# Performance work log

Hardware: AMD Instinct MI355X
Metric: run time of the kernel (lower is better)

## Reference

```python
import jax, jax.numpy as jnp
import numpy as np

B, J, O = 32, 20, 20
D, H, F, L = 256, 8, 1024, 6
S = J * O
DH = D // H
NL = L + 1  # 6 encoder blocks + final block stacked together


def setup_inputs() -> dict:
    ks = jax.random.split(jax.random.key(0), 16)
    s = 0.02
    am = jax.random.randint(ks[4], (B, J), 0, 2) == 1
    am = am.at[:, 0].set(False)  # at least one unmasked job per row (avoid all -inf softmax)
    return {
        "operations": jax.random.normal(ks[0], (B, J, O, 2), jnp.float32),
        "job_ops_mask": jax.random.normal(ks[1], (B, J, O, O), jnp.float32),
        "ops_machines_mask": jax.random.normal(ks[2], (B, S, S), jnp.float32),
        "jobs_next_op_idx": jax.random.randint(ks[3], (B, J, 1), 0, O),
        "action_mask": am,
        "qkv_w": jax.random.normal(ks[5], (NL, 3 * D, D), jnp.float32) * s,
        "qkv_b": jnp.zeros((NL, 3 * D), jnp.float32),
        "out_w": jax.random.normal(ks[6], (NL, D, D), jnp.float32) * s,
        "out_b": jnp.zeros((NL, D), jnp.float32),
        "ln1_g": jnp.ones((NL, D), jnp.float32),
        "ln1_b": jnp.zeros((NL, D), jnp.float32),
        "ln2_g": jnp.ones((NL, D), jnp.float32),
        "ln2_b": jnp.zeros((NL, D), jnp.float32),
        "ff1_w": jax.random.normal(ks[7], (NL, F, D), jnp.float32) * s,
        "ff1_b": jnp.zeros((NL, F), jnp.float32),
        "ff2_w": jax.random.normal(ks[8], (NL, D, F), jnp.float32) * s,
        "ff2_b": jnp.zeros((NL, D), jnp.float32),
        "op_emb_w": jax.random.normal(ks[9], (D, 2), jnp.float32) * s,
        "op_emb_b": jnp.zeros((D,), jnp.float32),
        "pol_w": jax.random.normal(ks[10], (1, D), jnp.float32) * s,
        "pol_b": jnp.zeros((1,), jnp.float32),
    }


def _ln(x, g, b):
    m = x.mean(-1, keepdims=True)
    v = ((x - m) ** 2).mean(-1, keepdims=True)
    return (x - m) * jax.lax.rsqrt(v + 1e-5) * g + b


def _mha(x, mask, qw, qb, ow, ob):
    N, Sq, _ = x.shape
    qkv = x @ qw.T + qb
    q, k, v = jnp.split(qkv, 3, axis=-1)
    q = q.reshape(N, Sq, H, DH).transpose(0, 2, 1, 3)
    k = k.reshape(N, Sq, H, DH).transpose(0, 2, 1, 3)
    v = v.reshape(N, Sq, H, DH).transpose(0, 2, 1, 3)
    sc = jnp.einsum("nhqd,nhkd->nhqk", q, k) / jnp.sqrt(jnp.float32(DH))
    sc = sc + mask  # additive float attn mask, broadcast over heads where needed
    a = jax.nn.softmax(sc, axis=-1)
    o = jnp.einsum("nhqk,nhkd->nhqd", a, v).transpose(0, 2, 1, 3).reshape(N, Sq, D)
    return o @ ow.T + ob


def _forward(operations, job_ops_mask, ops_machines_mask, jobs_next_op_idx, action_mask,
             qkv_w, qkv_b, out_w, out_b, ln1_g, ln1_b, ln2_g, ln2_b,
             ff1_w, ff1_b, ff2_w, ff2_b, op_emb_w, op_emb_b, pol_w, pol_b):
    def block(x, mask, i):  # pre-norm TransformerEncoderLayer, gelu, dropout=0
        h = _ln(x, ln1_g[i], ln1_b[i])
        x = x + _mha(h, mask, qkv_w[i], qkv_b[i], out_w[i], out_b[i])
        h = _ln(x, ln2_g[i], ln2_b[i])
        ff = jax.nn.gelu(h @ ff1_w[i].T + ff1_b[i], approximate=False) @ ff2_w[i].T + ff2_b[i]
        return x + ff

    # sinusoidal positional encoding over the operation index
    pos = jnp.arange(O, dtype=jnp.float32)[:, None]
    div = jnp.exp(jnp.arange(0, D, 2, dtype=jnp.float32) * (-np.log(10000.0) / D))
    pe = jnp.stack([jnp.sin(pos * div), jnp.cos(pos * div)], axis=-1).reshape(O, D)
    x = operations @ op_emb_w.T + op_emb_b + pe[None, None]  # (B,J,O,D)

    # ALiBi slopes: 1/x^(i+1), x = 256^(1/H)
    base = (2.0 ** 8) ** (1.0 / H)
    slope = (1.0 / base ** jnp.arange(1, H + 1, dtype=jnp.float32))[None, :, None, None]
    job_mask = job_ops_mask.reshape(B * J, 1, O, O) * slope  # (B*J, H, O, O)
    mach_mask = ops_machines_mask[:, None, :, :]  # (B, 1, S, S), identical across heads

    for i in range(L):
        if i % 2 == 0:  # per-job attention over operations
            x = block(x.reshape(B * J, O, D), job_mask, i).reshape(B, J, O, D)
        else:  # per-machine attention over all operations
            x = block(x.reshape(B, S, D), mach_mask, i).reshape(B, J, O, D)

    idx = jnp.broadcast_to(jobs_next_op_idx[:, :, :, None], (B, J, 1, D))
    nxt = jnp.take_along_axis(x, idx, axis=2)[:, :, 0, :]  # (B, J, D)
    kp = jnp.where(action_mask, -jnp.inf, 0.0)[:, None, None, :]  # key padding mask
    nxt = block(nxt, kp, L)
    logits = (nxt @ pol_w.T + pol_b)[:, :, 0]
    return jnp.where(action_mask, -jnp.inf, logits)


def reference(operations, job_ops_mask, ops_machines_mask, jobs_next_op_idx, action_mask,
              qkv_w, qkv_b, out_w, out_b, ln1_g, ln1_b, ln2_g, ln2_b,
              ff1_w, ff1_b, ff2_w, ff2_b, op_emb_w, op_emb_b, pol_w, pol_b):
    return _forward(operations, job_ops_mask, ops_machines_mask, jobs_next_op_idx, action_mask,
                    qkv_w, qkv_b, out_w, out_b, ln1_g, ln1_b, ln2_g, ln2_b,
                    ff1_w, ff1_b, ff2_w, ff2_b, op_emb_w, op_emb_b, pol_w, pol_b)
```

## Files before the change

kernel.cpp:

```cpp
#include <hip/hip_runtime.h>
#include <math.h>

#define B_  32
#define J_  20
#define O_  20
#define S_  400
#define D_  256
#define H_  8
#define F_  1024
#define L_  6
#define T_  12800
#define T2_ 640

#define NEG_BIG (-1e30f)

typedef __attribute__((ext_vector_type(8))) short short8;
typedef __attribute__((ext_vector_type(4))) float f32x4;

__device__ __forceinline__ short f2b(float f) {
  union { float f; unsigned u; } c; c.f = f;
  unsigned r = (c.u + 0x7FFFu + ((c.u >> 16) & 1u)) >> 16;
  return (short)r;
}
__device__ __forceinline__ float b2f(short s) {
  union { unsigned u; float f; } c;
  c.u = ((unsigned)(unsigned short)s) << 16;
  return c.f;
}
__device__ __forceinline__ unsigned addpk(unsigned a, unsigned b) {
  union { unsigned u; float f; } x, y;
  x.u = a << 16;        y.u = b << 16;        float lo = x.f + y.f;
  x.u = a & 0xffff0000u; y.u = b & 0xffff0000u; float hi = x.f + y.f;
  return (unsigned)(unsigned short)f2b(lo) | ((unsigned)(unsigned short)f2b(hi) << 16);
}
__device__ __forceinline__ void async_copy16(const short* g, short* l) {
  __builtin_amdgcn_global_load_lds(
      (const __attribute__((address_space(1))) void*)g,
      (__attribute__((address_space(3))) void*)l, 16, 0, 0);
}

__global__ __launch_bounds__(256) void k_f2b4(
    const float* __restrict__ s0, short* __restrict__ d0,
    const float* __restrict__ s1, short* __restrict__ d1,
    const float* __restrict__ s2, short* __restrict__ d2,
    const float* __restrict__ s3, short* __restrict__ d3,
    const float* __restrict__ s4, short* __restrict__ d4)
{
  int bid = blockIdx.x;
  const float* src; short* dst; int base;
  if (bid < 672)        { src = s0; dst = d0; base = bid; }
  else if (bid < 896)   { src = s1; dst = d1; base = bid - 672; }
  else if (bid < 1792)  { src = s2; dst = d2; base = bid - 896; }
  else if (bid < 2688)  { src = s3; dst = d3; base = bid - 1792; }
  else                  { src = s4; dst = d4; base = bid - 2688; }
  int i = (base * 256 + threadIdx.x) * 8;
  float4 a = *(const float4*)(src + i);
  float4 b = *(const float4*)(src + i + 4);
  short8 o;
  o[0] = f2b(a.x); o[1] = f2b(a.y); o[2] = f2b(a.z); o[3] = f2b(a.w);
  o[4] = f2b(b.x); o[5] = f2b(b.y); o[6] = f2b(b.z); o[7] = f2b(b.w);
  *(short8*)(dst + i) = o;
}

__global__ __launch_bounds__(640) void k_maskconv(
    const void* __restrict__ am_raw, int* __restrict__ am_out)
{
  __shared__ int isInt32;
  const int tid = threadIdx.x;
  if (tid == 0) isInt32 = 1;
  __syncthreads();
  if (tid < 160) {
    int v = ((const int*)am_raw)[tid];
    if (v != 0 && v != 1) atomicAnd(&isInt32, 0);
  }
  __syncthreads();
  if (tid < 640) {
    int v;
    if (isInt32) v = ((const int*)am_raw)[tid] != 0;
    else         v = ((const unsigned char*)am_raw)[tid] != 0;
    am_out[tid] = v;
  }
}

__global__ __launch_bounds__(256) void k_embed(
    const float* __restrict__ ops, const float* __restrict__ ew,
    const float* __restrict__ eb, short* __restrict__ x)
{
  int idx = blockIdx.x * 256 + threadIdx.x;
  int d = idx & 255;
  int t = idx >> 8;
  int o = t % O_;
  float a0 = ops[(size_t)t * 2 + 0], a1 = ops[(size_t)t * 2 + 1];
  int k = d >> 1;
  float div = expf((float)(2 * k) * -0.03597789207803197f);
  float ang = (float)o * div;
  float pe = (d & 1) ? cosf(ang) : sinf(ang);
  x[idx] = f2b(a0 * ew[d * 2 + 0] + a1 * ew[d * 2 + 1] + eb[d] + pe);
}

__global__ __launch_bounds__(256) void k_ln(
    const short* __restrict__ x, const float* __restrict__ g, const float* __restrict__ b,
    short* __restrict__ out, int nTok)
{
  int gid = blockIdx.x * 256 + threadIdx.x;
  int tok = gid >> 6, lane = threadIdx.x & 63;
  if (tok >= nTok) return;
  int2 pk = ((const int2*)(x + (size_t)tok * 256))[lane];
  union { unsigned u; float f; } c;
  float vx, vy, vz, vw;
  c.u = (unsigned)pk.x << 16;        vx = c.f;
  c.u = (unsigned)pk.x & 0xffff0000u; vy = c.f;
  c.u = (unsigned)pk.y << 16;        vz = c.f;
  c.u = (unsigned)pk.y & 0xffff0000u; vw = c.f;
  float s = vx + vy + vz + vw;
  #pragma unroll
  for (int off = 32; off > 0; off >>= 1) s += __shfl_down(s, off);
  float mean = __shfl(s, 0) * (1.f / 256.f);
  float dx = vx - mean, dy = vy - mean, dz = vz - mean, dw = vw - mean;
  float q = dx * dx + dy * dy + dz * dz + dw * dw;
  #pragma unroll
  for (int off = 32; off > 0; off >>= 1) q += __shfl_down(q, off);
  float var = __shfl(q, 0) * (1.f / 256.f);
  float inv = 1.f / sqrtf(var + 1e-5f);
  float4 gv = ((const float4*)g)[lane];
  float4 bv = ((const float4*)b)[lane];
  float ox = dx * inv * gv.x + bv.x;
  float oy = dy * inv * gv.y + bv.y;
  float oz = dz * inv * gv.z + bv.z;
  float ow = dw * inv * gv.w + bv.w;
  int2 po;
  po.x = (int)(unsigned short)f2b(ox) | ((int)(unsigned short)f2b(oy) << 16);
  po.y = (int)(unsigned short)f2b(oz) | ((int)(unsigned short)f2b(ow) << 16);
  ((int2*)(out + (size_t)tok * 256))[lane] = po;
}

__global__ __launch_bounds__(256) void k_gemm_bf16(
    const short* __restrict__ A, const short* __restrict__ W,
    const float* __restrict__ bias, const short* __restrict__ R,
    short* __restrict__ C, int M, int N, int K, int act)
{
  __shared__ short LDS_[32768];
  short* Csf = LDS_;
  const int tid  = threadIdx.x;
  const int lane = tid & 63;
  const int wv   = tid >> 6;
  const int lm   = lane & 15;
  const int quad = lane >> 4;
  const int wm   = (wv >> 1) * 64;
  const int wn   = (wv & 1) * 64;
  const int n0 = blockIdx.x * 128;
  const int m0 = blockIdx.y * 128;

  f32x4 acc[4][4] = {};

#define GB_STAGE(buf, kk)                                                      \
  { _Pragma("unroll")                                                          \
    for (int i = 0; i < 4; ++i) {                                              \
      const int c    = tid + 256 * i;                       \
      const int row  = c >> 3;                                     \
      const int kc8  = ((c & 7) ^ (row & 7)) * 8;                              \
      async_copy16(A + (size_t)(m0 + row) * K + (kk) + kc8,                    \
                   &LDS_[(buf) * 16384 + c * 8]);                              \
      async_copy16(W + (size_t)(n0 + row) * K + (kk) + kc8,                    \
                   &LDS_[(buf) * 16384 + 8192 + c * 8]);                       \
    } }

  GB_STAGE(0, 0)
  __syncthreads();

  const int nIter = K >> 6;
  for (int t = 0; t < nIter; ++t) {
    const int cur = t & 1;
    if (t + 1 < nIter) GB_STAGE(cur ^ 1, (t + 1) << 6)
    const short* Asf = &LDS_[cur * 16384];
    const short* Bsf = &LDS_[cur * 16384 + 8192];
    #pragma unroll
    for (int kh = 0; kh < 2; ++kh) {
      short8 af[4], bf[4];
      #pragma unroll
      for (int i = 0; i < 4; ++i) {
        const int row  = wm + i * 16 + lm;
        const int slot = (kh * 4 + quad) ^ (lm & 7);
        af[i] = *(short8*)&Asf[(row * 8 + slot) * 8];
      }
      #pragma unroll
      for (int j = 0; j < 4; ++j) {
        const int row  = wn + j * 16 + lm;
        const int slot = (kh * 4 + quad) ^ (lm & 7);
        bf[j] = *(short8*)&Bsf[(row * 8 + slot) * 8];
      }
      #pragma unroll
      for (int i = 0; i < 4; ++i)
        #pragma unroll
        for (int j = 0; j < 4; ++j)
          acc[i][j] = __builtin_amdgcn_mfma_f32_16x16x32_bf16(af[i], bf[j], acc[i][j], 0, 0, 0);
    }
    __syncthreads();
  }
#undef GB_STAGE

  #pragma unroll
  for (int j = 0; j < 4; ++j) {
    const int ccol = wn + j * 16 + lm;
    const float bv = bias[n0 + ccol];
    #pragma unroll
    for (int i = 0; i < 4; ++i) {
      #pragma unroll
      for (int r = 0; r < 4; ++r) {
        const int row = wm + i * 16 + quad * 4 + r;
        float vvv = acc[i][j][r] + bv;
        if (act) vvv = vvv / (1.f + __expf(-1.702f * vvv));
        Csf[row * 136 + ccol] = f2b(vvv);
      }
    }
  }
  __syncthreads();
  {
    const int srow = tid >> 1, sh = (tid & 1) * 64;
    const size_t gbase = (size_t)(m0 + srow) * N + n0 + sh;
    const short* ls = &Csf[srow * 136 + sh];
    #pragma unroll
    for (int u = 0; u < 8; ++u) {
      uint4 v = *(const uint4*)(ls + u * 8);
      if (R) {
        uint4 rv = *(const uint4*)(R + gbase + u * 8);
        v.x = addpk(v.x, rv.x); v.y = addpk(v.y, rv.y);
        v.z = addpk(v.z, rv.z); v.w = addpk(v.w, rv.w);
      }
      *(uint4*)(C + gbase + u * 8) = v;
    }
  }
}

__global__ __launch_bounds__(256) void k_gemm_ln(
    const short* __restrict__ A, const short* __restrict__ W,
    const float* __restrict__ bias, const short* __restrict__ R,
    short* __restrict__ X, short* __restrict__ Hout,
    const float* __restrict__ g, const float* __restrict__ bb_,
    int M, int K)
{
  __shared__ short LDS_[40960];
  short* Csf = LDS_;
  const int tid  = threadIdx.x;
  const int lane = tid & 63;
  const int wv   = tid >> 6;
  const int lm   = lane & 15;
  const int quad = lane >> 4;
  const int wn   = wv * 64;
  const int m0   = blockIdx.x * 64;

  f32x4 acc[4][4] = {};

#define GL_STAGE(buf, kk)                                                      \
  { _Pragma("unroll")                                                          \
    for (int i = 0; i < 2; ++i) {                           \
      const int c   = tid + 256 * i;                                           \
      const int row = c >> 3;                                                  \
      const int kc8 = ((c & 7) ^ (row & 7)) * 8;                               \
      async_copy16(A + (size_t)(m0 + row) * K + (kk) + kc8,                    \
                   &LDS_[(buf) * 20480 + c * 8]);                              \
    }                                                                          \
    _Pragma("unroll")                                                          \
    for (int i = 0; i < 8; ++i) {           \
      const int c   = tid + 256 * i;                                           \
      const int row = c >> 3;                                                  \
      const int kc8 = ((c & 7) ^ (row & 7)) * 8;                               \
      async_copy16(W + (size_t)row * K + (kk) + kc8,                           \
                   &LDS_[(buf) * 20480 + 4096 + c * 8]);                       \
    } }

  GL_STAGE(0, 0)
  __syncthreads();

  const int nIter = K >> 6;
  for (int t = 0; t < nIter; ++t) {
    const int cur = t & 1;
    if (t + 1 < nIter) GL_STAGE(cur ^ 1, (t + 1) << 6)
    const short* Asf = &LDS_[cur * 20480];
    const short* Bsf = &LDS_[cur * 20480 + 4096];
    #pragma unroll
    for (int kh = 0; kh < 2; ++kh) {
      short8 af[4], bf[4];
      #pragma unroll
      for (int i = 0; i < 4; ++i) {
        const int row  = i * 16 + lm;
        const int slot = (kh * 4 + quad) ^ (lm & 7);
        af[i] = *(short8*)&Asf[(row * 8 + slot) * 8];
      }
      #pragma unroll
      for (int j = 0; j < 4; ++j) {
        const int row  = wn + j * 16 + lm;
        const int slot = (kh * 4 + quad) ^ (lm & 7);
        bf[j] = *(short8*)&Bsf[(row * 8 + slot) * 8];
      }
      #pragma unroll
      for (int i = 0; i < 4; ++i)
        #pragma unroll
        for (int j = 0; j < 4; ++j)
          acc[i][j] = __builtin_amdgcn_mfma_f32_16x16x32_bf16(af[i], bf[j], acc[i][j], 0, 0, 0);
    }
    __syncthreads();
  }
#undef GL_STAGE

  #pragma unroll
  for (int j = 0; j < 4; ++j) {
    const int ccol = wn + j * 16 + lm;
    const float bv = bias[ccol];
    #pragma unroll
    for (int i = 0; i < 4; ++i) {
      #pragma unroll
      for (int r = 0; r < 4; ++r) {
        const int row = i * 16 + quad * 4 + r;
        Csf[row * 264 + ccol] = f2b(acc[i][j][r] + bv);
      }
    }
  }
  __syncthreads();

  {
    const int row = tid >> 2, cb = (tid & 3) * 64;
    const size_t gbase = (size_t)(m0 + row) * 256 + cb;
    const short* ls = &Csf[row * 264 + cb];
    uint4 xv[8];
    float s1 = 0.f, s2 = 0.f;
    #pragma unroll
    for (int u = 0; u < 8; ++u) {
      uint4 v = *(const uint4*)(ls + u * 8);
      uint4 rv = *(const uint4*)(R + gbase + u * 8);
      v.x = addpk(v.x, rv.x); v.y = addpk(v.y, rv.y);
      v.z = addpk(v.z, rv.z); v.w = addpk(v.w, rv.w);
      xv[u] = v;
      *(uint4*)(X + gbase + u * 8) = v;
      #pragma unroll
      for (int w2 = 0; w2 < 4; ++w2) {
        unsigned pv = (&v.x)[w2];
        union { unsigned u; float f; } c1, c2;
        c1.u = pv << 16; c2.u = pv & 0xffff0000u;
        s1 += c1.f + c2.f;
        s2 += c1.f * c1.f + c2.f * c2.f;
      }
    }
    s1 += __shfl_xor(s1, 1); s2 += __shfl_xor(s2, 1);
    s1 += __shfl_xor(s1, 2); s2 += __shfl_xor(s2, 2);
    const float mean = s1 * (1.f / 256.f);
    const float var  = s2 * (1.f / 256.f) - mean * mean;
    const float inv  = 1.f / sqrtf(var + 1e-5f);
    #pragma unroll
    for (int u = 0; u < 8; ++u) {
      float4 g0 = *(const float4*)(g + cb + u * 8);
      float4 g1 = *(const float4*)(g + cb + u * 8 + 4);
      float4 b0 = *(const float4*)(bb_ + cb + u * 8);
      float4 b1 = *(const float4*)(bb_ + cb + u * 8 + 4);
      auto lnpk = [&](unsigned pv, float ga, float gb2, float ba, float bb2) -> unsigned {
        union { unsigned u; float f; } c1, c2;
        c1.u = pv << 16; c2.u = pv & 0xffff0000u;
        float lo = (c1.f - mean) * inv * ga + ba;
        float hi = (c2.f - mean) * inv * gb2 + bb2;
        return (unsigned)(unsigned short)f2b(lo) | ((unsigned)(unsigned short)f2b(hi) << 16);
      };
      uint4 hv;
      hv.x = lnpk(xv[u].x, g0.x, g0.y, b0.x, b0.y);
      hv.y = lnpk(xv[u].y, g0.z, g0.w, b0.z, b0.w);
      hv.z = lnpk(xv[u].z, g1.x, g1.y, b1.x, b1.y);
      hv.w = lnpk(xv[u].w, g1.z, g1.w, b1.z, b1.w);
      *(uint4*)(Hout + gbase + u * 8) = hv;
    }
  }
}

#define QSTR 776
#define PSTR20 40
__global__ __launch_bounds__(512) void k_attn20_mfma(
    const short* __restrict__ qkv, short* __restrict__ att,
    const float* __restrict__ jmask, const int* __restrict__ amask, int mode)
{
  __shared__ short QK[32 * QSTR];
  __shared__ short Ps[8][32 * PSTR20];
  const int seq  = blockIdx.x;
  const int tid  = threadIdx.x;
  const int wv   = tid >> 6;
  const int lane = tid & 63;
  const int l15  = lane & 15;
  const int quad = lane >> 4;
  const float scale = 0.1767766952966369f;

  for (int e = tid; e < 3072; e += 512) {
    int row = e / 96, c8 = (e % 96) * 8;
    uint4 v = {0u, 0u, 0u, 0u};
    if (row < 20) v = *(const uint4*)(qkv + ((size_t)seq * 20 + row) * 768 + c8);
    *(uint4*)&QK[row * QSTR + c8] = v;
  }
  __syncthreads();

  const short8 aq0 = *(short8*)&QK[(0  + l15) * QSTR + wv * 32 + quad * 8];
  const short8 aq1 = *(short8*)&QK[(16 + l15) * QSTR + wv * 32 + quad * 8];
  const short8 bk0 = *(short8*)&QK[(0  + l15) * QSTR + 256 + wv * 32 + quad * 8];
  const short8 bk1 = *(short8*)&QK[(16 + l15) * QSTR + 256 + wv * 32 + quad * 8];
  f32x4 z4 = {0.f, 0.f, 0.f, 0.f};
  f32x4 s00 = __builtin_amdgcn_mfma_f32_16x16x32_bf16(aq0, bk0, z4, 0, 0, 0);
  f32x4 s01 = __builtin_amdgcn_mfma_f32_16x16x32_bf16(aq0, bk1, z4, 0, 0, 0);
  f32x4 s10 = __builtin_amdgcn_mfma_f32_16x16x32_bf16(aq1, bk0, z4, 0, 0, 0);
  f32x4 s11 = __builtin_amdgcn_mfma_f32_16x16x32_bf16(aq1, bk1, z4, 0, 0, 0);

  const float slope = exp2f(-(float)(wv + 1));
  short* psw = &Ps[wv][0];
  float l0[4] = {0.f, 0.f, 0.f, 0.f};
  float l1[4] = {0.f, 0.f, 0.f, 0.f};

  #pragma unroll
  for (int kt = 0; kt < 2; ++kt) {
    const int k  = kt * 16 + l15;
    const int kc = (k < 20) ? k : 19;
    float madd1 = 0.f;
    if (mode == 1) madd1 = amask[seq * 20 + kc] ? NEG_BIG : 0.f;
    #pragma unroll
    for (int qt = 0; qt < 2; ++qt) {
      f32x4 s = (kt == 0) ? (qt == 0 ? s00 : s10) : (qt == 0 ? s01 : s11);
      #pragma unroll
      for (int r = 0; r < 4; ++r) {
        const int q  = qt * 16 + quad * 4 + r;
        const int qc = (q < 20) ? q : 19;
        float sv = s[r] * scale;
        if (mode == 0) sv += jmask[(size_t)seq * 400 + qc * 20 + kc] * slope;
        else           sv += madd1;
        float p = (k < 20) ? __expf(fminf(sv, 40.f)) : 0.f;
        if (qt == 0) l0[r] += p; else l1[r] += p;
        psw[q * PSTR20 + k] = f2b(p);
      }
    }
  }
  #pragma unroll
  for (int r = 0; r < 4; ++r) {
    float t0 = l0[r];
    t0 += __shfl_xor(t0, 1); t0 += __shfl_xor(t0, 2);
    t0 += __shfl_xor(t0, 4); t0 += __shfl_xor(t0, 8);
    l0[r] = 1.f / t0;
    float t1 = l1[r];
    t1 += __shfl_xor(t1, 1); t1 += __shfl_xor(t1, 2);
    t1 += __shfl_xor(t1, 4); t1 += __shfl_xor(t1, 8);
    l1[r] = 1.f / t1;
  }

  const short8 pf0 = *(short8*)&psw[(0  + l15) * PSTR20 + quad * 8];
  const short8 pf1 = *(short8*)&psw[(16 + l15) * PSTR20 + quad * 8];
  #pragma unroll
  for (int dt = 0; dt < 2; ++dt) {
    const int d = wv * 32 + dt * 16 + l15;
    short8 vf;
    #pragma unroll
    for (int j = 0; j < 8; ++j)
      vf[j] = QK[(quad * 8 + j) * QSTR + 512 + d];
    f32x4 o0 = __builtin_amdgcn_mfma_f32_16x16x32_bf16(pf0, vf, z4, 0, 0, 0);
    f32x4 o1 = __builtin_amdgcn_mfma_f32_16x16x32_bf16(pf1, vf, z4, 0, 0, 0);
    #pragma unroll
    for (int r = 0; r < 4; ++r) {
      const int q = quad * 4 + r;
      att[((size_t)seq * 20 + q) * 256 + d] = f2b(o0[r] * l0[r]);
    }
    if (quad == 0) {
      #pragma unroll
      for (int r = 0; r < 4; ++r) {
        const int q = 16 + r;
        att[((size_t)seq * 20 + q) * 256 + d] = f2b(o1[r] * l1[r]);
      }
    }
  }
}

#define VTS 416
__global__ __launch_bounds__(256) void k_vtrans(
    const short* __restrict__ qkv, short* __restrict__ vt)
{
  __shared__ short T[64][73];
  const int bid = blockIdx.x;
  const int b  = bid / 28, rem = bid % 28;
  const int kt = rem / 4, dt = rem % 4;
  const int k0 = kt * 64, d0 = dt * 64;
  const int tid = threadIdx.x;
  #pragma unroll
  for (int i = 0; i < 2; ++i) {
    const int c = tid + 256 * i;
    const int row = c >> 3, cc = (c & 7) * 8;
    const int tok = k0 + row;
    uint4 v = {0u, 0u, 0u, 0u};
    if (tok < 400)
      v = *(const uint4*)(qkv + ((size_t)(b * 400 + tok)) * 768 + 512 + d0 + cc);
    *(uint4*)&T[row][cc] = v;
  }
  __syncthreads();
  #pragma unroll
  for (int i = 0; i < 2; ++i) {
    const int c = tid + 256 * i;
    const int dl = c >> 3, kk = (c & 7) * 8;
    if (k0 + kk < VTS) {
      short8 o;
      #pragma unroll
      for (int j = 0; j < 8; ++j) o[j] = T[kk + j][dl];
      *(short8*)(vt + ((size_t)(b * 256 + d0 + dl)) * VTS + k0 + kk) = o;
    }
  }
}

#define KSTR  36
#define VSTRL 436
#define PSTRW 40
__global__ __launch_bounds__(512) void k_attn400_mfma(
    const short* __restrict__ qkv, const short* __restrict__ vt,
    short* __restrict__ att, const short* __restrict__ mbf)
{
  __shared__ short Kl[416 * KSTR];
  __shared__ short Vl[32 * VSTRL];
  __shared__ short Pl[8][2 * 16 * PSTRW];

  const int id   = blockIdx.x;
  const int b    = id & 31;
  const int hd   = id >> 5;
  const int tid  = threadIdx.x;
  const int wv   = tid >> 6;
  const int lane = tid & 63;
  const int l15  = lane & 15;
  const int quad = lane >> 4;
  const float scale = 0.1767766952966369f;

  const short* qbase = qkv + (size_t)b * 400 * 768;
  const short* kgl   = qbase + 256 + hd * 32;
  const short* vtb   = vt + ((size_t)b * 256 + hd * 32) * VTS;

  for (int e = tid; e < 1664; e += 512) {
    const int row = e >> 2, seg = e & 3;
    const int rs = row < 400 ? row : 399;
    uint4 v = *(const uint4*)(kgl + (size_t)rs * 768 + seg * 8);
    *(uint4*)&Kl[row * KSTR + seg * 8] = v;
  }
  for (int e = tid; e < 1664; e += 512) {
    const int row = e / 52, seg = e % 52;
    uint4 v = *(const uint4*)(vtb + (size_t)row * VTS + seg * 8);
    *(uint4*)&Vl[row * VSTRL + seg * 8] = v;
  }
  __syncthreads();

  short* Pw0 = &Pl[wv][0];
  short* Pw1 = &Pl[wv][16 * PSTRW];

  for (int tile = wv; tile < 13; tile += 8) {
    const int q0 = tile * 32;
    const short8 af0 = *(const short8*)(qbase + (size_t)(q0 + l15) * 768 + hd * 32 + quad * 8);
    int aq1 = q0 + 16 + l15; if (aq1 > 399) aq1 = 399;
    const short8 af1 = *(const short8*)(qbase + (size_t)aq1 * 768 + hd * 32 + quad * 8);
    const short* mr0 = mbf + (size_t)(b * 400 + q0 + l15) * 400;
    const short* mr1 = mbf + (size_t)(b * 400 + aq1) * 400;

    f32x4 accO[2][2] = {};
    float lsum0 = 0.f, lsum1 = 0.f;

    #pragma unroll
    for (int k0 = 0; k0 < 416; k0 += 32) {
      const short8 kf0 = *(const short8*)&Kl[(k0 + l15) * KSTR + quad * 8];
      const short8 kf1 = *(const short8*)&Kl[(k0 + 16 + l15) * KSTR + quad * 8];
      f32x4 z4 = {0.f, 0.f, 0.f, 0.f};
      f32x4 s00 = __builtin_amdgcn_mfma_f32_16x16x32_bf16(kf0, af0, z4, 0, 0, 0);
      f32x4 s01 = __builtin_amdgcn_mfma_f32_16x16x32_bf16(kf1, af0, z4, 0, 0, 0);
      f32x4 s10 = __builtin_amdgcn_mfma_f32_16x16x32_bf16(kf0, af1, z4, 0, 0, 0);
      f32x4 s11 = __builtin_amdgcn_mfma_f32_16x16x32_bf16(kf1, af1, z4, 0, 0, 0);

      uint2 ma0 = *(const uint2*)(mr0 + k0 + quad * 4);
      uint2 mb0 = *(const uint2*)(mr0 + k0 + 16 + quad * 4);
      uint2 ma1 = *(const uint2*)(mr1 + k0 + quad * 4);
      uint2 mb1 = *(const uint2*)(mr1 + k0 + 16 + quad * 4);

      float p00[4], p01[4], p10[4], p11[4];
      #pragma unroll
      for (int r = 0; r < 4; ++r) {
        const int kB = k0 + 16 + quad * 4 + r;
        union { unsigned u; float f; } cm;
        unsigned wa0 = (r < 2) ? ma0.x : ma0.y;
        unsigned wb0 = (r < 2) ? mb0.x : mb0.y;
        unsigned wa1 = (r < 2) ? ma1.x : ma1.y;
        unsigned wb1 = (r < 2) ? mb1.x : mb1.y;
        cm.u = (r & 1) ? (wa0 & 0xffff0000u) : (wa0 << 16); float mA0 = cm.f;
        cm.u = (r & 1) ? (wb0 & 0xffff0000u) : (wb0 << 16); float mB0 = cm.f;
        cm.u = (r & 1) ? (wa1 & 0xffff0000u) : (wa1 << 16); float mA1 = cm.f;
        cm.u = (r & 1) ? (wb1 & 0xffff0000u) : (wb1 << 16); float mB1 = cm.f;
        float sA0 = s00[r] * scale + mA0;
        float sB0 = (kB < 400) ? (s01[r] * scale + mB0) : NEG_BIG;
        float sA1 = s10[r] * scale + mA1;
        float sB1 = (kB < 400) ? (s11[r] * scale + mB1) : NEG_BIG;
        p00[r] = __expf(fminf(sA0, 40.f));
        p01[r] = __expf(fminf(sB0, 40.f));
        p10[r] = __expf(fminf(sA1, 40.f));
        p11[r] = __expf(fminf(sB1, 40.f));
        lsum0 += p00[r] + p01[r];
        lsum1 += p10[r] + p11[r];
      }

      unsigned q00, q01, q02, q03, q10, q11, q12, q13;
      asm("v_cvt_pk_bf16_f32 %0, %1, %2" : "=v"(q00) : "v"(p00[0]), "v"(p00[1]));
      asm("v_cvt_pk_bf16_f32 %0, %1, %2" : "=v"(q01) : "v"(p00[2]), "v"(p00[3]));
      asm("v_cvt_pk_bf16_f32 %0, %1, %2" : "=v"(q02) : "v"(p01[0]), "v"(p01[1]));
      asm("v_cvt_pk_bf16_f32 %0, %1, %2" : "=v"(q03) : "v"(p01[2]), "v"(p01[3]));
      asm("v_cvt_pk_bf16_f32 %0, %1, %2" : "=v"(q10) : "v"(p10[0]), "v"(p10[1]));
      asm("v_cvt_pk_bf16_f32 %0, %1, %2" : "=v"(q11) : "v"(p10[2]), "v"(p10[3]));
      asm("v_cvt_pk_bf16_f32 %0, %1, %2" : "=v"(q12) : "v"(p11[0]), "v"(p11[1]));
      asm("v_cvt_pk_bf16_f32 %0, %1, %2" : "=v"(q13) : "v"(p11[2]), "v"(p11[3]));
      uint2 w00; w00.x = q00; w00.y = q01;
      uint2 w01; w01.x = q02; w01.y = q03;
      uint2 w10; w10.x = q10; w10.y = q11;
      uint2 w11; w11.x = q12; w11.y = q13;
      *(uint2*)&Pw0[l15 * PSTRW + quad * 4]      = w00;
      *(uint2*)&Pw0[l15 * PSTRW + 16 + quad * 4] = w01;
      *(uint2*)&Pw1[l15 * PSTRW + quad * 4]      = w10;
      *(uint2*)&Pw1[l15 * PSTRW + 16 + quad * 4] = w11;
      const short8 pf0 = *(short8*)&Pw0[l15 * PSTRW + quad * 8];
      const short8 pf1 = *(short8*)&Pw1[l15 * PSTRW + quad * 8];

      const short8 vf0 = *(const short8*)&Vl[l15 * VSTRL + k0 + quad * 8];
      const short8 vf1 = *(const short8*)&Vl[(16 + l15) * VSTRL + k0 + quad * 8];
      accO[0][0] = __builtin_amdgcn_mfma_f32_16x16x32_bf16(vf0, pf0, accO[0][0], 0, 0, 0);
      accO[0][1] = __builtin_amdgcn_mfma_f32_16x16x32_bf16(vf1, pf0, accO[0][1], 0, 0, 0);
      accO[1][0] = __builtin_amdgcn_mfma_f32_16x16x32_bf16(vf0, pf1, accO[1][0], 0, 0, 0);
      accO[1][1] = __builtin_amdgcn_mfma_f32_16x16x32_bf16(vf1, pf1, accO[1][1], 0, 0, 0);
    }

    lsum0 += __shfl_xor(lsum0, 16);
    lsum0 += __shfl_xor(lsum0, 32);
    lsum1 += __shfl_xor(lsum1, 16);
    lsum1 += __shfl_xor(lsum1, 32);
    const float inv0 = 1.f / lsum0;
    const float inv1 = 1.f / lsum1;

    #pragma unroll
    for (int qh = 0; qh < 2; ++qh) {
      const int q = q0 + qh * 16 + l15;
      if (q >= 400) continue;
      const float inv = qh ? inv1 : inv0;
      #pragma unroll
      for (int c = 0; c < 2; ++c) {
        float a0 = accO[qh][c][0] * inv, a1 = accO[qh][c][1] * inv;
        float a2 = accO[qh][c][2] * inv, a3 = accO[qh][c][3] * inv;
        unsigned o01, o23;
        asm("v_cvt_pk_bf16_f32 %0, %1, %2" : "=v"(o01) : "v"(a0), "v"(a1));
        asm("v_cvt_pk_bf16_f32 %0, %1, %2" : "=v"(o23) : "v"(a2), "v"(a3));
        uint2 ov; ov.x = o01; ov.y = o23;
        *(uint2*)&att[((size_t)b * 400 + q) * 256 + hd * 32 + c * 16 + quad * 4] = ov;
      }
    }
  }
}

__global__ __launch_bounds__(256) void k_gather2(
    const short* __restrict__ x, const short* __restrict__ h,
    const int* __restrict__ idx, short* __restrict__ x2, short* __restrict__ h2)
{
  int t = blockIdx.x * 256 + threadIdx.x;
  if (t >= 640 * 16) return;
  int bj = t >> 4, c = t & 15;
  int o = idx[bj];
  size_t src = ((size_t)bj * 20 + o) * 256;
  ((uint4*)(x2 + (size_t)bj * 256))[c] = ((const uint4*)(x + src))[c];
  ((uint4*)(h2 + (size_t)bj * 256))[c] = ((const uint4*)(h + src))[c];
}

__global__ __launch_bounds__(256) void k_logits(
    const short* __restrict__ x2, const float* __restrict__ pw, const float* __restrict__ pb,
    const int* __restrict__ am, float* __restrict__ out)
{
  int gid = blockIdx.x * 256 + threadIdx.x;
  int row = gid >> 6, lane = threadIdx.x & 63;
  int2 pk = ((const int2*)(x2 + (size_t)row * 256))[lane];
  union { unsigned u; float f; } c;
  float vx, vy, vz, vw;
  c.u = (unsigned)pk.x << 16;         vx = c.f;
  c.u = (unsigned)pk.x & 0xffff0000u; vy = c.f;
  c.u = (unsigned)pk.y << 16;         vz = c.f;
  c.u = (unsigned)pk.y & 0xffff0000u; vw = c.f;
  float4 w = ((const float4*)pw)[lane];
  float s = vx * w.x + vy * w.y + vz * w.z + vw * w.w;
  #pragma unroll
  for (int off = 32; off > 0; off >>= 1) s += __shfl_down(s, off);
  if (lane == 0) out[row] = am[row] ? NEG_BIG : (s + pb[0]);
}

extern "C" void kernel_launch(void* const* d_in, const int* in_sizes, int n_in,
                              void* d_out, int out_size, void* d_ws, size_t ws_size,
                              hipStream_t stream)
{
  (void)in_sizes; (void)n_in; (void)out_size; (void)ws_size;
  const float* operations        = (const float*)d_in[0];
  const float* job_ops_mask      = (const float*)d_in[1];
  const float* ops_machines_mask = (const float*)d_in[2];
  const int*   jobs_next_op_idx  = (const int*)d_in[3];
  const void*  action_mask_raw   = (const void*)d_in[4];
  const float* qkv_w = (const float*)d_in[5];
  const float* qkv_b = (const float*)d_in[6];
  const float* out_w = (const float*)d_in[7];
  const float* out_b = (const float*)d_in[8];
  const float* ln1_g = (const float*)d_in[9];
  const float* ln1_b = (const float*)d_in[10];
  const float* ln2_g = (const float*)d_in[11];
  const float* ln2_b = (const float*)d_in[12];
  const float* ff1_w = (const float*)d_in[13];
  const float* ff1_b = (const float*)d_in[14];
  const float* ff2_w = (const float*)d_in[15];
  const float* ff2_b = (const float*)d_in[16];
  const float* op_emb_w = (const float*)d_in[17];
  const float* op_emb_b = (const float*)d_in[18];
  const float* pol_w = (const float*)d_in[19];
  const float* pol_b = (const float*)d_in[20];
  float* out = (float*)d_out;

  short* x    = (short*)d_ws;
  short* x2   = x + (size_t)T_ * D_;
  short* h    = x2 + (size_t)T2_ * D_;
  short* big  = h + (size_t)T_ * D_;
  short* h2   = big + (size_t)T_ * F_;
  short* big2 = h2 + (size_t)T2_ * D_;
  int*   amc  = (int*)(big2 + (size_t)T2_ * F_);
  short* bwq  = (short*)(amc + 640);
  short* bwo  = bwq + (size_t)7 * 768 * 256;
  short* bwf1 = bwo + (size_t)7 * 256 * 256;
  short* bwf2 = bwf1 + (size_t)7 * 1024 * 256;
  short* mbf  = bwf2 + (size_t)7 * 256 * 1024;
  short* vt   = mbf + (size_t)B_ * 400 * 400;

  auto gemm = [&](const short* A, const short* Wb, const float* bias, const short* R,
                  short* C, int M, int N, int K, int act) {
    k_gemm_bf16<<<dim3(N / 128, M / 128), dim3(256), 0, stream>>>(
        A, Wb, bias, R, C, M, N, K, act);
  };
  auto gemm_ln = [&](const short* A, const short* Wb, const float* bias, const short* R,
                     short* X, short* Hout, const float* g, const float* b, int M, int K) {
    k_gemm_ln<<<dim3(M / 64), dim3(256), 0, stream>>>(
        A, Wb, bias, R, X, Hout, g, b, M, K);
  };

  k_f2b4<<<dim3(5188), 256, 0, stream>>>(qkv_w, bwq, out_w, bwo, ff1_w, bwf1,
                                         ff2_w, bwf2, ops_machines_mask, mbf);
  k_maskconv<<<dim3(1), dim3(640), 0, stream>>>(action_mask_raw, amc);
  k_embed<<<dim3(T_ * D_ / 256), dim3(256), 0, stream>>>(operations, op_emb_w, op_emb_b, x);
  k_ln<<<dim3(T_ / 4), 256, 0, stream>>>(x, ln1_g, ln1_b, h, T_);

  for (int i = 0; i < L_; ++i) {
    const short* qw  = bwq  + (size_t)i * 768 * 256;
    const float* qb  = qkv_b + (size_t)i * 768;
    const short* ow  = bwo  + (size_t)i * 256 * 256;
    const float* ob  = out_b + (size_t)i * 256;
    const short* f1w = bwf1 + (size_t)i * 1024 * 256;
    const float* f1b = ff1_b + (size_t)i * 1024;
    const short* f2w = bwf2 + (size_t)i * 256 * 1024;
    const float* f2b_ = ff2_b + (size_t)i * 256;
    gemm(h, qw, qb, nullptr, big, T_, 768, 256, 0);
    if ((i & 1) == 0) {
      k_attn20_mfma<<<dim3(640), 512, 0, stream>>>(big, h, job_ops_mask, nullptr, 0);
    } else {
      k_vtrans<<<dim3(896), 256, 0, stream>>>(big, vt);
      k_attn400_mfma<<<dim3(256), 512, 0, stream>>>(big, vt, h, mbf);
    }
    gemm_ln(h, ow, ob, x, x, h, ln2_g + i * D_, ln2_b + i * D_, T_, 256);
    gemm(h, f1w, f1b, nullptr, big, T_, 1024, 256, 1);
    gemm_ln(big, f2w, f2b_, x, x, h, ln1_g + (i + 1) * D_, ln1_b + (i + 1) * D_, T_, 1024);
  }

  k_gather2<<<dim3(40), 256, 0, stream>>>(x, h, jobs_next_op_idx, x2, h2);

  {
    int i = L_;
    const short* qw  = bwq  + (size_t)i * 768 * 256;
    const float* qb  = qkv_b + (size_t)i * 768;
    const short* ow  = bwo  + (size_t)i * 256 * 256;
    const float* ob  = out_b + (size_t)i * 256;
    const short* f1w = bwf1 + (size_t)i * 1024 * 256;
    const float* f1b = ff1_b + (size_t)i * 1024;
    const short* f2w = bwf2 + (size_t)i * 256 * 1024;
    const float* f2b_ = ff2_b + (size_t)i * 256;
    gemm(h2, qw, qb, nullptr, big2, T2_, 768, 256, 0);
    k_attn20_mfma<<<dim3(32), 512, 0, stream>>>(big2, h2, nullptr, amc, 1);
    gemm_ln(h2, ow, ob, x2, x2, h2, ln2_g + i * D_, ln2_b + i * D_, T2_, 256);
    gemm(h2, f1w, f1b, nullptr, big2, T2_, 1024, 256, 1);
    gemm(big2, f2w, f2b_, x2, x2, T2_, 256, 1024, 0);
  }

  k_logits<<<dim3(160), 256, 0, stream>>>(x2, pol_w, pol_b, amc, out);
}
```

Measured before the change: 868.4 us.

## Fuse V transpose into attention, embed with LN, mask conversion into weight cast

Removes the separate V-transpose kernel: the 400-token attention kernel now reads V straight from the QKV buffer and transposes it into shared memory with scalar stores. The embedding and first layer norm become one kernel, and action-mask conversion runs as an extra block of the weight-conversion kernel. This cuts several launches and the global write and read of the transposed V buffer. The price is slower scattered 2-byte shared-memory stores, with possible bank conflicts, during the attention load phase.

Result: no change. 856.0 us (-1.4%).

```diff
diff --git a/kernel.cpp b/kernel.cpp
--- a/kernel.cpp
+++ b/kernel.cpp
@@ -44,9 +44,28 @@
     const float* __restrict__ s1, short* __restrict__ d1,
     const float* __restrict__ s2, short* __restrict__ d2,
     const float* __restrict__ s3, short* __restrict__ d3,
-    const float* __restrict__ s4, short* __restrict__ d4)
+    const float* __restrict__ s4, short* __restrict__ d4,
+    const void* __restrict__ am_raw, int* __restrict__ am_out)
 {
   int bid = blockIdx.x;
+  if (bid == 5188) {
+    __shared__ int isInt32;
+    const int tid = threadIdx.x;
+    if (tid == 0) isInt32 = 1;
+    __syncthreads();
+    if (tid < 160) {
+      int v = ((const int*)am_raw)[tid];
+      if (v != 0 && v != 1) atomicAnd(&isInt32, 0);
+    }
+    __syncthreads();
+    for (int e = tid; e < 640; e += 256) {
+      int v;
+      if (isInt32) v = ((const int*)am_raw)[e] != 0;
+      else         v = ((const unsigned char*)am_raw)[e] != 0;
+      am_out[e] = v;
+    }
+    return;
+  }
   const float* src; short* dst; int base;
   if (bid < 672)        { src = s0; dst = d0; base = bid; }
   else if (bid < 896)   { src = s1; dst = d1; base = bid - 672; }
@@ -62,56 +81,33 @@
   *(short8*)(dst + i) = o;
 }
 
-__global__ __launch_bounds__(640) void k_maskconv(
-    const void* __restrict__ am_raw, int* __restrict__ am_out)
-{
-  __shared__ int isInt32;
-  const int tid = threadIdx.x;
-  if (tid == 0) isInt32 = 1;
-  __syncthreads();
-  if (tid < 160) {
-    int v = ((const int*)am_raw)[tid];
-    if (v != 0 && v != 1) atomicAnd(&isInt32, 0);
-  }
-  __syncthreads();
-  if (tid < 640) {
-    int v;
-    if (isInt32) v = ((const int*)am_raw)[tid] != 0;
-    else         v = ((const unsigned char*)am_raw)[tid] != 0;
-    am_out[tid] = v;
-  }
-}
-
-__global__ __launch_bounds__(256) void k_embed(
+__global__ __launch_bounds__(256) void k_embed_ln(
     const float* __restrict__ ops, const float* __restrict__ ew,
-    const float* __restrict__ eb, short* __restrict__ x)
-{
-  int idx = blockIdx.x * 256 + threadIdx.x;
-  int d = idx & 255;
-  int t = idx >> 8;
-  int o = t % O_;
-  float a0 = ops[(size_t)t * 2 + 0], a1 = ops[(size_t)t * 2 + 1];
-  int k = d >> 1;
-  float div = expf((float)(2 * k) * -0.03597789207803197f);
-  float ang = (float)o * div;
-  float pe = (d & 1) ? cosf(ang) : sinf(ang);
-  x[idx] = f2b(a0 * ew[d * 2 + 0] + a1 * ew[d * 2 + 1] + eb[d] + pe);
-}
-
-__global__ __launch_bounds__(256) void k_ln(
-    const short* __restrict__ x, const float* __restrict__ g, const float* __restrict__ b,
-    short* __restrict__ out, int nTok)
+    const float* __restrict__ eb, const float* __restrict__ g,
+    const float* __restrict__ b, short* __restrict__ x, short* __restrict__ h)
 {
   int gid = blockIdx.x * 256 + threadIdx.x;
   int tok = gid >> 6, lane = threadIdx.x & 63;
-  if (tok >= nTok) return;
-  int2 pk = ((const int2*)(x + (size_t)tok * 256))[lane];
-  union { unsigned u; float f; } c;
-  float vx, vy, vz, vw;
-  c.u = (unsigned)pk.x << 16;        vx = c.f;
-  c.u = (unsigned)pk.x & 0xffff0000u; vy = c.f;
-  c.u = (unsigned)pk.y << 16;        vz = c.f;
-  c.u = (unsigned)pk.y & 0xffff0000u; vw = c.f;
+  int o = tok % O_;
+  float a0 = ops[(size_t)tok * 2 + 0], a1 = ops[(size_t)tok * 2 + 1];
+  const int d0 = lane * 4;
+  float4 e0 = *(const float4*)(ew + d0 * 2);
+  float4 e1 = *(const float4*)(ew + d0 * 2 + 4);
+  float4 ebv = *(const float4*)(eb + d0);
+  const float cc = -0.03597789207803197f;
+  float div0 = expf((float)d0 * cc);
+  float div1 = expf((float)(d0 + 2) * cc);
+  float ang0 = (float)o * div0, ang1 = (float)o * div1;
+  float vx = a0 * e0.x + a1 * e0.y + ebv.x + sinf(ang0);
+  float vy = a0 * e0.z + a1 * e0.w + ebv.y + cosf(ang0);
+  float vz = a0 * e1.x + a1 * e1.y + ebv.z + sinf(ang1);
+  float vw = a0 * e1.z + a1 * e1.w + ebv.w + cosf(ang1);
+
+  int2 px;
+  px.x = (int)(unsigned short)f2b(vx) | ((int)(unsigned short)f2b(vy) << 16);
+  px.y = (int)(unsigned short)f2b(vz) | ((int)(unsigned short)f2b(vw) << 16);
+  ((int2*)(x + (size_t)tok * 256))[lane] = px;
+
   float s = vx + vy + vz + vw;
   #pragma unroll
   for (int off = 32; off > 0; off >>= 1) s += __shfl_down(s, off);
@@ -131,7 +127,7 @@
   int2 po;
   po.x = (int)(unsigned short)f2b(ox) | ((int)(unsigned short)f2b(oy) << 16);
   po.y = (int)(unsigned short)f2b(oz) | ((int)(unsigned short)f2b(ow) << 16);
-  ((int2*)(out + (size_t)tok * 256))[lane] = po;
+  ((int2*)(h + (size_t)tok * 256))[lane] = po;
 }
 
 __global__ __launch_bounds__(256) void k_gemm_bf16(
@@ -468,46 +464,12 @@
   }
 }
 
-#define VTS 416
-__global__ __launch_bounds__(256) void k_vtrans(
-    const short* __restrict__ qkv, short* __restrict__ vt)
-{
-  __shared__ short T[64][73];
-  const int bid = blockIdx.x;
-  const int b  = bid / 28, rem = bid % 28;
-  const int kt = rem / 4, dt = rem % 4;
-  const int k0 = kt * 64, d0 = dt * 64;
-  const int tid = threadIdx.x;
-  #pragma unroll
-  for (int i = 0; i < 2; ++i) {
-    const int c = tid + 256 * i;
-    const int row = c >> 3, cc = (c & 7) * 8;
-    const int tok = k0 + row;
-    uint4 v = {0u, 0u, 0u, 0u};
-    if (tok < 400)
-      v = *(const uint4*)(qkv + ((size_t)(b * 400 + tok)) * 768 + 512 + d0 + cc);
-    *(uint4*)&T[row][cc] = v;
-  }
-  __syncthreads();
-  #pragma unroll
-  for (int i = 0; i < 2; ++i) {
-    const int c = tid + 256 * i;
-    const int dl = c >> 3, kk = (c & 7) * 8;
-    if (k0 + kk < VTS) {
-      short8 o;
-      #pragma unroll
-      for (int j = 0; j < 8; ++j) o[j] = T[kk + j][dl];
-      *(short8*)(vt + ((size_t)(b * 256 + d0 + dl)) * VTS + k0 + kk) = o;
-    }
-  }
-}
-
 #define KSTR  36
 #define VSTRL 436
 #define PSTRW 40
 __global__ __launch_bounds__(512) void k_attn400_mfma(
-    const short* __restrict__ qkv, const short* __restrict__ vt,
-    short* __restrict__ att, const short* __restrict__ mbf)
+    const short* __restrict__ qkv, short* __restrict__ att,
+    const short* __restrict__ mbf)
 {
   __shared__ short Kl[416 * KSTR];
   __shared__ short Vl[32 * VSTRL];
@@ -525,7 +487,7 @@
 
   const short* qbase = qkv + (size_t)b * 400 * 768;
   const short* kgl   = qbase + 256 + hd * 32;
-  const short* vtb   = vt + ((size_t)b * 256 + hd * 32) * VTS;
+  const short* vgl   = qbase + 512 + hd * 32;
 
   for (int e = tid; e < 1664; e += 512) {
     const int row = e >> 2, seg = e & 3;
@@ -534,9 +496,18 @@
     *(uint4*)&Kl[row * KSTR + seg * 8] = v;
   }
   for (int e = tid; e < 1664; e += 512) {
-    const int row = e / 52, seg = e % 52;
-    uint4 v = *(const uint4*)(vtb + (size_t)row * VTS + seg * 8);
-    *(uint4*)&Vl[row * VSTRL + seg * 8] = v;
+    const int row = e >> 2, seg = e & 3;
+    const int rs = row < 400 ? row : 399;
+    uint4 v = *(const uint4*)(vgl + (size_t)rs * 768 + seg * 8);
+    const int dbase = seg * 8;
+    Vl[(dbase + 0) * VSTRL + row] = (short)(v.x & 0xffff);
+    Vl[(dbase + 1) * VSTRL + row] = (short)(v.x >> 16);
+    Vl[(dbase + 2) * VSTRL + row] = (short)(v.y & 0xffff);
+    Vl[(dbase + 3) * VSTRL + row] = (short)(v.y >> 16);
+    Vl[(dbase + 4) * VSTRL + row] = (short)(v.z & 0xffff);
+    Vl[(dbase + 5) * VSTRL + row] = (short)(v.z >> 16);
+    Vl[(dbase + 6) * VSTRL + row] = (short)(v.w & 0xffff);
+    Vl[(dbase + 7) * VSTRL + row] = (short)(v.w >> 16);
   }
   __syncthreads();
 
@@ -721,7 +692,6 @@
   short* bwf1 = bwo + (size_t)7 * 256 * 256;
   short* bwf2 = bwf1 + (size_t)7 * 1024 * 256;
   short* mbf  = bwf2 + (size_t)7 * 256 * 1024;
-  short* vt   = mbf + (size_t)B_ * 400 * 400;
 
   auto gemm = [&](const short* A, const short* Wb, const float* bias, const short* R,
                   short* C, int M, int N, int K, int act) {
@@ -734,11 +704,11 @@
         A, Wb, bias, R, X, Hout, g, b, M, K);
   };
 
-  k_f2b4<<<dim3(5188), 256, 0, stream>>>(qkv_w, bwq, out_w, bwo, ff1_w, bwf1,
-                                         ff2_w, bwf2, ops_machines_mask, mbf);
-  k_maskconv<<<dim3(1), dim3(640), 0, stream>>>(action_mask_raw, amc);
-  k_embed<<<dim3(T_ * D_ / 256), dim3(256), 0, stream>>>(operations, op_emb_w, op_emb_b, x);
-  k_ln<<<dim3(T_ / 4), 256, 0, stream>>>(x, ln1_g, ln1_b, h, T_);
+  k_f2b4<<<dim3(5189), 256, 0, stream>>>(qkv_w, bwq, out_w, bwo, ff1_w, bwf1,
+                                         ff2_w, bwf2, ops_machines_mask, mbf,
+                                         action_mask_raw, amc);
+  k_embed_ln<<<dim3(T_ / 4), 256, 0, stream>>>(operations, op_emb_w, op_emb_b,
+                                               ln1_g, ln1_b, x, h);
 
   for (int i = 0; i < L_; ++i) {
     const short* qw  = bwq  + (size_t)i * 768 * 256;
@@ -753,8 +723,7 @@
     if ((i & 1) == 0) {
       k_attn20_mfma<<<dim3(640), 512, 0, stream>>>(big, h, job_ops_mask, nullptr, 0);
     } else {
-      k_vtrans<<<dim3(896), 256, 0, stream>>>(big, vt);
-      k_attn400_mfma<<<dim3(256), 512, 0, stream>>>(big, vt, h, mbf);
+      k_attn400_mfma<<<dim3(256), 512, 0, stream>>>(big, h, mbf);
     }
     gemm_ln(h, ow, ob, x, x, h, ln2_g + i * D_, ln2_b + i * D_, T_, 256);
     gemm(h, f1w, f1b, nullptr, big, T_, 1024, 256, 1);
```
